# Optimization experiments

Measured on AMD Instinct MI355X. Metric: run time of the kernel, lower is better.

The kernel has to match this reference:

```python
import jax, jax.numpy as jnp
import numpy as np

N_EMBD = 2048
QKV_EMBD = 2048
N_HEAD = 32
N_KV_HEAD = 8
HEAD_DIM = QKV_EMBD // N_HEAD  # 64
GROUPS = N_HEAD // N_KV_HEAD   # 4
ROPE_THETA = 10000.0
SCALE = float(np.sqrt(HEAD_DIM))


def setup_inputs() -> dict:
    key = jax.random.key(0)
    ks = jax.random.split(key, 12)
    B, S = 2, 2048
    inp = {
        "query": jax.random.normal(ks[0], (B, S, N_EMBD), jnp.float32),
        "key": jax.random.normal(ks[1], (B, S, N_EMBD), jnp.float32),
        "value": jax.random.normal(ks[2], (B, S, N_EMBD), jnp.float32),
        "mask": jnp.ones((B, S), dtype=bool),
        "Wq": jax.random.normal(ks[3], (QKV_EMBD, N_EMBD), jnp.float32) * 0.02,
        "bq": jnp.zeros((QKV_EMBD,), jnp.float32),
        "Wk": jax.random.normal(ks[4], (N_KV_HEAD * HEAD_DIM, N_EMBD), jnp.float32) * 0.02,
        "bk": jnp.zeros((N_KV_HEAD * HEAD_DIM,), jnp.float32),
        "Wv": jax.random.normal(ks[5], (N_KV_HEAD * HEAD_DIM, N_EMBD), jnp.float32) * 0.02,
        "bv": jnp.zeros((N_KV_HEAD * HEAD_DIM,), jnp.float32),
        "Wo": jax.random.normal(ks[6], (N_EMBD, QKV_EMBD), jnp.float32) * 0.02,
        "bo": jnp.zeros((N_EMBD,), jnp.float32),
    }
    return inp


def _rotate_half(x):
    d = x.shape[-1] // 2
    return jnp.concatenate([-x[..., d:], x[..., :d]], axis=-1)


def _rope_cos_sin(seq_len, dtype):
    # rope_factor == 1.0 -> no NTK adjustment; is_causal -> position_ids = arange
    inv_freq = 1.0 / (ROPE_THETA ** (jnp.arange(0, HEAD_DIM, 2, dtype=jnp.float32) / HEAD_DIM))
    pos = jnp.arange(seq_len, dtype=jnp.float32)
    freqs = jnp.einsum("i,j->ij", pos, inv_freq)           # [S, D/2]
    emb = jnp.concatenate([freqs, freqs], axis=-1)          # [S, D]
    return jnp.cos(emb).astype(dtype)[None, None], jnp.sin(emb).astype(dtype)[None, None]


def reference(query, key, value, mask, Wq, bq, Wk, bk, Wv, bv, Wo, bo):
    B, S, _ = query.shape
    Q = (query @ Wq.T + bq).reshape(B, S, N_HEAD, HEAD_DIM).transpose(0, 2, 1, 3)      # [B,H,S,D]
    K = (key @ Wk.T + bk).reshape(B, S, N_KV_HEAD, HEAD_DIM).transpose(0, 2, 1, 3)     # [B,KV,S,D]
    V = (value @ Wv.T + bv).reshape(B, S, N_KV_HEAD, HEAD_DIM).transpose(0, 2, 1, 3)

    cos, sin = _rope_cos_sin(S, Q.dtype)
    Q = Q * cos + _rotate_half(Q) * sin
    K = K * cos + _rotate_half(K) * sin

    # interleaved GQA repeat: each kv head serves GROUPS consecutive query heads
    K = jnp.repeat(K, GROUPS, axis=1)  # [B,H,S,D]
    V = jnp.repeat(V, GROUPS, axis=1)

    attn = jnp.einsum("bhqd,bhkd->bhqk", Q, K)              # [B,H,S,S]
    causal = jnp.tril(jnp.ones((S, S), dtype=bool))
    full_mask = mask[:, None, None, :] & causal[None, None]  # [B,1,S,S]
    attn = jnp.where(full_mask, attn, jnp.finfo(attn.dtype).min)
    attn_weights = jax.nn.softmax(attn / SCALE, axis=-1)     # dropout p=0 (eval)
    out = jnp.einsum("bhqk,bhkd->bhqd", attn_weights, V)
    out = out.transpose(0, 2, 1, 3).reshape(B, S, QKV_EMBD)
    return out @ Wo.T + bo
```

## Files before the change

### kernel.cpp

```cpp
#include <hip/hip_runtime.h>
#include <hip/hip_bf16.h>
#include <cmath>

#define NE   2048
#define NH   32
#define NKV  8
#define HD   64
#define SEQ  2048
#define NB   2

typedef __attribute__((ext_vector_type(4))) float f32x4;
typedef __attribute__((ext_vector_type(16))) float f32x16;
typedef __attribute__((ext_vector_type(8))) short bf16x8;
typedef __attribute__((ext_vector_type(4))) short bf16x4;
typedef __attribute__((ext_vector_type(4))) unsigned u32x4;

typedef const __attribute__((address_space(1))) void cgvoid;
typedef __attribute__((address_space(3))) void lvoid;

#define QSCALE 0.18033688011112042f

__device__ __forceinline__ short f2bf(float f) {
  union { float f; unsigned u; } v; v.f = f;
  unsigned r = v.u + 0x7fffu + ((v.u >> 16) & 1u);
  return (short)(r >> 16);
}

__device__ __forceinline__ unsigned cvt_pk_bf16(float a, float b) {
  unsigned r;
  asm("v_cvt_pk_bf16_f32 %0, %1, %2" : "=v"(r) : "v"(a), "v"(b));
  return r;
}

__global__ __launch_bounds__(256) void cvt_w(
    const float* __restrict__ s0, short* __restrict__ d0,
    const float* __restrict__ s1, short* __restrict__ d1,
    const float* __restrict__ s2, short* __restrict__ d2,
    const float* __restrict__ s3, short* __restrict__ d3)
{
  int idx = blockIdx.x * 256 + threadIdx.x;
  const float* s; short* d; int rel;
  if      (idx < 524288)  { s = s0; d = d0; rel = idx; }
  else if (idx < 655360)  { s = s1; d = d1; rel = idx - 524288; }
  else if (idx < 786432)  { s = s2; d = d2; rel = idx - 655360; }
  else                    { s = s3; d = d3; rel = idx - 786432; }
  size_t off = (size_t)rel * 8;
  f32x4 a = *(const f32x4*)(s + off);
  f32x4 b = *(const f32x4*)(s + off + 4);
  bf16x8 o;
  #pragma unroll
  for (int j = 0; j < 4; ++j) { o[j] = f2bf(a[j]); o[4 + j] = f2bf(b[j]); }
  *(bf16x8*)(d + off) = o;
}

template<int EPI>
__device__ __forceinline__ void gemm256_body(
    short* As, short* Ws, int m0, int n0,
    const float* __restrict__ A, const short* __restrict__ W,
    const float* __restrict__ bias, void* __restrict__ Cout, int K)
{
  const int t = threadIdx.x, lane = t & 63, w = t >> 6;
  const int lr = lane & 15, lg = lane >> 4;
  const int wm = (w >> 2) * 128, wn = (w & 3) * 64;

  f32x4 acc[8][4];
  #pragma unroll
  for (int i = 0; i < 8; ++i)
    #pragma unroll
    for (int j = 0; j < 4; ++j) acc[i][j] = (f32x4){0.f, 0.f, 0.f, 0.f};

  auto STAGE_W = [&](int kt) {
    const int k0 = kt << 6;
    short* Wd = Ws + (kt & 1) * 16384;
    #pragma unroll
    for (int it = 0; it < 4; ++it) {
      int e = it * 512 + t, r = e >> 3, c = e & 7;
      int cs = ((c ^ (r & 7)) << 3);
      __builtin_amdgcn_global_load_lds((cgvoid*)(W + (size_t)(n0 + r) * K + k0 + cs),
                                       (lvoid*)(Wd + e * 8), 16, 0, 0);
    }
  };

  f32x4 areg[4][2];
  auto LOAD_A = [&](int kt) {
    const int k0 = kt << 6;
    #pragma unroll
    for (int it = 0; it < 4; ++it) {
      int e = it * 512 + t, r = e >> 3, c = e & 7;
      int cs = ((c ^ (r & 7)) << 3);
      const float* src = A + (size_t)(m0 + r) * K + k0 + cs;
      areg[it][0] = *(const f32x4*)(src);
      areg[it][1] = *(const f32x4*)(src + 4);
    }
  };
  auto WRITE_A = [&](int kt) {
    short* Ad = As + (kt & 1) * 16384;
    #pragma unroll
    for (int it = 0; it < 4; ++it) {
      int e = it * 512 + t;
      u32x4 v;
      v[0] = cvt_pk_bf16(areg[it][0][0], areg[it][0][1]);
      v[1] = cvt_pk_bf16(areg[it][0][2], areg[it][0][3]);
      v[2] = cvt_pk_bf16(areg[it][1][0], areg[it][1][1]);
      v[3] = cvt_pk_bf16(areg[it][1][2], areg[it][1][3]);
      *(u32x4*)(Ad + e * 8) = v;
    }
  };

  const int nt = K >> 6;

  STAGE_W(0);
  LOAD_A(0);
  WRITE_A(0);
  asm volatile("s_waitcnt lgkmcnt(0)" ::: "memory");

  for (int ti = 0; ti < nt; ++ti) {
    const short* Ab = As + (ti & 1) * 16384;
    const short* Wb = Ws + (ti & 1) * 16384;
    if (ti + 1 < nt) {
      STAGE_W(ti + 1);
      LOAD_A(ti + 1);
      asm volatile("s_waitcnt vmcnt(12)" ::: "memory");
    } else {
      asm volatile("s_waitcnt vmcnt(0)" ::: "memory");
    }
    __builtin_amdgcn_s_barrier();

    bf16x8 wf[2][4];
    #pragma unroll
    for (int ks = 0; ks < 2; ++ks)
      #pragma unroll
      for (int nf = 0; nf < 4; ++nf) {
        int row = wn + nf * 16 + lr;
        wf[ks][nf] = *(const bf16x8*)(Wb + row * 64 + (((ks * 4 + lg) ^ (row & 7)) << 3));
      }
    #pragma unroll
    for (int mq = 0; mq < 4; ++mq) {
      bf16x8 af[2][2];
      #pragma unroll
      for (int ks = 0; ks < 2; ++ks)
        #pragma unroll
        for (int mi = 0; mi < 2; ++mi) {
          int row = wm + (mq * 2 + mi) * 16 + lr;
          af[ks][mi] = *(const bf16x8*)(Ab + row * 64 + (((ks * 4 + lg) ^ (row & 7)) << 3));
        }
      __builtin_amdgcn_s_setprio(1);
      #pragma unroll
      for (int ks = 0; ks < 2; ++ks)
        #pragma unroll
        for (int mi = 0; mi < 2; ++mi)
          #pragma unroll
          for (int nf = 0; nf < 4; ++nf)
            acc[mq * 2 + mi][nf] =
                __builtin_amdgcn_mfma_f32_16x16x32_bf16(af[ks][mi], wf[ks][nf],
                                                        acc[mq * 2 + mi][nf], 0, 0, 0);
      __builtin_amdgcn_s_setprio(0);
    }
    if (ti + 1 < nt) WRITE_A(ti + 1);
    asm volatile("s_waitcnt lgkmcnt(0)" ::: "memory");
    __builtin_amdgcn_s_barrier();
  }

  if (EPI == 1) {
    short* C = (short*)Cout;
    #pragma unroll
    for (int mf = 0; mf < 8; ++mf)
      #pragma unroll
      for (int nf = 0; nf < 4; ++nf) {
        int n = n0 + wn + nf * 16 + lr;
        int kv = n >> 6, d = n & 63;
        int mb = m0 + wm + mf * 16 + lg * 4;
        int b = mb >> 11, s = mb & (SEQ - 1);
        bf16x4 pb;
        #pragma unroll
        for (int i = 0; i < 4; ++i) pb[i] = f2bf(acc[mf][nf][i] + bias[n]);
        *(bf16x4*)(C + (((size_t)b * NKV + kv) * HD + d) * SEQ + s) = pb;
      }
  } else {
    const int HN = (EPI == 2) ? NH : NKV;
    short* C = (short*)Cout;
    #pragma unroll
    for (int mf = 0; mf < 8; ++mf)
      #pragma unroll
      for (int nf2 = 0; nf2 < 2; ++nf2) {
        int n1 = n0 + wn + nf2 * 16 + lr;
        int d1 = n1 & 63;
        int h = n1 >> 6;
        float inv = exp2f(-(float)d1 * (13.287712379549449f / 32.0f));
        #pragma unroll
        for (int i = 0; i < 4; ++i) {
          int m = m0 + wm + mf * 16 + lg * 4 + i;
          int b = m >> 11, s = m & (SEQ - 1);
          float v1 = acc[mf][nf2][i] + bias[n1];
          float v2 = acc[mf][nf2 + 2][i] + bias[n1 + 32];
          float ang = (float)s * inv;
          float c, sn;
          __sincosf(ang, &sn, &c);
          float o1 = v1 * c - v2 * sn;
          float o2 = v2 * c + v1 * sn;
          if (EPI == 2) { o1 *= QSCALE; o2 *= QSCALE; }
          size_t base = (((size_t)b * HN + h) * SEQ + s) * HD;
          C[base + d1]      = f2bf(o1);
          C[base + d1 + 32] = f2bf(o2);
        }
      }
  }
}

__global__ __launch_bounds__(512, 2) void gemm_qkv256(
    const float* __restrict__ qA, const short* __restrict__ Wq,
    const float* __restrict__ bq, short* __restrict__ Qout,
    const float* __restrict__ kA, const short* __restrict__ Wk,
    const float* __restrict__ bk, short* __restrict__ Kout,
    const float* __restrict__ vA, const short* __restrict__ Wv,
    const float* __restrict__ bv, short* __restrict__ Vout)
{
  __shared__ __align__(16) short As[2 * 256 * 64];
  __shared__ __align__(16) short Ws[2 * 256 * 64];
  int orig = blockIdx.x;
  int bid = (orig & 7) * 24 + (orig >> 3);
  if (bid < 128) {
    gemm256_body<2>(As, Ws, (bid & 15) * 256, (bid >> 4) * 256, qA, Wq, bq, (void*)Qout, NE);
  } else if (bid < 160) {
    int b2 = bid - 128;
    gemm256_body<3>(As, Ws, (b2 & 15) * 256, (b2 >> 4) * 256, kA, Wk, bk, (void*)Kout, NE);
  } else {
    int b2 = bid - 160;
    gemm256_body<1>(As, Ws, (b2 & 15) * 256, (b2 >> 4) * 256, vA, Wv, bv, (void*)Vout, NE);
  }
}

__global__ __launch_bounds__(256) void gemm_o(
    const short* __restrict__ A, const short* __restrict__ W,
    const float* __restrict__ bias, float* __restrict__ C, int N, int K)
{
  __shared__ __align__(16) short As[2 * 128 * 64];
  __shared__ __align__(16) short Ws[2 * 128 * 64];
  const int t = threadIdx.x, lane = t & 63, w = t >> 6;
  const int lr = lane & 15, lg = lane >> 4;
  const int wm = (w >> 1) * 64, wn = (w & 1) * 64;
  const int L = blockIdx.x;
  const int xcd = L & 7, slot = L >> 3;
  const int bx = xcd + 8 * (slot >> 4);
  const int byy = slot & 15;
  const int m0 = bx * 128, n0 = byy * 128;

  f32x4 acc[4][4];
  #pragma unroll
  for (int i = 0; i < 4; ++i)
    #pragma unroll
    for (int j = 0; j < 4; ++j) acc[i][j] = (f32x4){0.f, 0.f, 0.f, 0.f};

  const int nt = K >> 6;
  #pragma unroll
  for (int it = 0; it < 4; ++it) {
    int e = it * 256 + t, r = e >> 3, c = e & 7;
    int cs = ((c ^ (r & 7)) << 3);
    __builtin_amdgcn_global_load_lds((cgvoid*)(A + (size_t)(m0 + r) * K + cs),
                                     (lvoid*)(As + e * 8), 16, 0, 0);
    __builtin_amdgcn_global_load_lds((cgvoid*)(W + (size_t)(n0 + r) * K + cs),
                                     (lvoid*)(Ws + e * 8), 16, 0, 0);
  }

  for (int ti = 0; ti < nt; ++ti) {
    const int cur = ti & 1;
    const short* Ab = As + cur * 8192;
    const short* Wb = Ws + cur * 8192;
    if (ti + 1 < nt) {
      const int k0 = (ti + 1) << 6;
      short* An = As + (cur ^ 1) * 8192;
      short* Wn = Ws + (cur ^ 1) * 8192;
      #pragma unroll
      for (int it = 0; it < 4; ++it) {
        int e = it * 256 + t, r = e >> 3, c = e & 7;
        int cs = ((c ^ (r & 7)) << 3);
        __builtin_amdgcn_global_load_lds((cgvoid*)(A + (size_t)(m0 + r) * K + k0 + cs),
                                         (lvoid*)(An + e * 8), 16, 0, 0);
        __builtin_amdgcn_global_load_lds((cgvoid*)(W + (size_t)(n0 + r) * K + k0 + cs),
                                         (lvoid*)(Wn + e * 8), 16, 0, 0);
      }
      asm volatile("s_waitcnt vmcnt(8)" ::: "memory");
    } else {
      asm volatile("s_waitcnt vmcnt(0)" ::: "memory");
    }
    __builtin_amdgcn_s_barrier();
    __builtin_amdgcn_sched_barrier(0);

    bf16x8 wf[2][4];
    #pragma unroll
    for (int ks = 0; ks < 2; ++ks)
      #pragma unroll
      for (int nf = 0; nf < 4; ++nf) {
        int row = wn + nf * 16 + lr;
        wf[ks][nf] = *(const bf16x8*)(Wb + row * 64 + (((ks * 4 + lg) ^ (row & 7)) << 3));
      }
    #pragma unroll
    for (int mq = 0; mq < 2; ++mq) {
      bf16x8 af[2][2];
      #pragma unroll
      for (int ks = 0; ks < 2; ++ks)
        #pragma unroll
        for (int mi = 0; mi < 2; ++mi) {
          int row = wm + (mq * 2 + mi) * 16 + lr;
          af[ks][mi] = *(const bf16x8*)(Ab + row * 64 + (((ks * 4 + lg) ^ (row & 7)) << 3));
        }
      __builtin_amdgcn_s_setprio(1);
      #pragma unroll
      for (int ks = 0; ks < 2; ++ks)
        #pragma unroll
        for (int mi = 0; mi < 2; ++mi)
          #pragma unroll
          for (int nf = 0; nf < 4; ++nf)
            acc[mq * 2 + mi][nf] =
                __builtin_amdgcn_mfma_f32_16x16x32_bf16(af[ks][mi], wf[ks][nf],
                                                        acc[mq * 2 + mi][nf], 0, 0, 0);
      __builtin_amdgcn_s_setprio(0);
      __builtin_amdgcn_s_barrier();
      __builtin_amdgcn_sched_barrier(0);
    }
  }

  #pragma unroll
  for (int mf = 0; mf < 4; ++mf)
    #pragma unroll
    for (int nf = 0; nf < 4; ++nf)
      #pragma unroll
      for (int i = 0; i < 4; ++i) {
        int m = m0 + wm + mf * 16 + lg * 4 + i;
        int n = n0 + wn + nf * 16 + lr;
        C[(size_t)m * N + n] = acc[mf][nf][i] + bias[n];
      }
}

__global__ __launch_bounds__(256) void attn_kernel(
    const short* __restrict__ Q, const short* __restrict__ K,
    const short* __restrict__ Vt, short* __restrict__ O)
{
  __shared__ __align__(16) short Ks[2][64 * 64];
  __shared__ __align__(16) short Vs[2][64 * 64];

  const int t = threadIdx.x, lane = t & 63, w = t >> 6;
  const int l31 = lane & 31, hi = lane >> 5;
  const int L = blockIdx.x;
  const int xcd = L & 7, slot = L >> 3;
  const int by = xcd + 8 * (slot >> 5);
  const int bx = slot & 31;
  const int b = by >> 3, kvh = by & 7;
  const int h = kvh * 4 + w;

  const short* Qh = Q + ((size_t)b * NH + h) * SEQ * HD;
  const short* Kh = K + ((size_t)b * NKV + kvh) * SEQ * HD;
  const short* Vh = Vt + ((size_t)b * NKV + kvh) * (size_t)HD * SEQ;

  #pragma unroll 1
  for (int pass = 0; pass < 2; ++pass) {
    const int qb32 = pass ? bx : (63 - bx);
    const int q0 = qb32 * 32;
    const int ntile = (qb32 >> 1) + 1;
    const int qpos = q0 + l31;

    bf16x8 qfr[4];
    #pragma unroll
    for (int dd = 0; dd < 4; ++dd)
      qfr[dd] = *(const bf16x8*)(Qh + (size_t)(q0 + l31) * HD + dd * 16 + hi * 8);

    f32x16 o[2];
    #pragma unroll
    for (int dh = 0; dh < 2; ++dh)
      #pragma unroll
      for (int r = 0; r < 16; ++r) o[dh][r] = 0.f;
    float lsum = 0.f;

    #pragma unroll
    for (int it = 0; it < 2; ++it) {
      int cid = it * 256 + t;
      int r = cid >> 3, c = cid & 7;
      int cs = ((c ^ (r & 7)) << 3);
      __builtin_amdgcn_global_load_lds((cgvoid*)(Kh + (size_t)r * HD + cs),
                                       (lvoid*)(Ks[0] + cid * 8), 16, 0, 0);
      __builtin_amdgcn_global_load_lds((cgvoid*)(Vh + (size_t)r * SEQ + cs),
                                       (lvoid*)(Vs[0] + cid * 8), 16, 0, 0);
    }
    __syncthreads();

    for (int ti = 0; ti < ntile; ++ti) {
      const int cur = ti & 1;
      if (ti + 1 < ntile) {
        const int kvn = (ti + 1) * 64;
        #pragma unroll
        for (int it = 0; it < 2; ++it) {
          int cid = it * 256 + t;
          int r = cid >> 3, c = cid & 7;
          int cs = ((c ^ (r & 7)) << 3);
          __builtin_amdgcn_global_load_lds((cgvoid*)(Kh + (size_t)(kvn + r) * HD + cs),
                                           (lvoid*)(Ks[cur ^ 1] + cid * 8), 16, 0, 0);
          __builtin_amdgcn_global_load_lds((cgvoid*)(Vh + (size_t)r * SEQ + kvn + cs),
                                           (lvoid*)(Vs[cur ^ 1] + cid * 8), 16, 0, 0);
        }
      }
      const int kv0 = ti * 64;
      const short* Kb = Ks[cur];
      const short* Vb = Vs[cur];

      f32x16 p[2];
      __builtin_amdgcn_s_setprio(1);
      #pragma unroll
      for (int f = 0; f < 2; ++f) {
        f32x16 z;
        #pragma unroll
        for (int r = 0; r < 16; ++r) z[r] = 0.f;
        #pragma unroll
        for (int dd = 0; dd < 4; ++dd) {
          int row = f * 32 + l31;
          bf16x8 ka = *(const bf16x8*)(Kb + row * 64 + (((2 * dd + hi) ^ (row & 7)) << 3));
          z = __builtin_amdgcn_mfma_f32_32x32x16_bf16(ka, qfr[dd], z, 0, 0, 0);
        }
        p[f] = z;
      }
      __builtin_amdgcn_s_setprio(0);

      if (ti == ntile - 1) {
        #pragma unroll
        for (int f = 0; f < 2; ++f)
          #pragma unroll
          for (int r = 0; r < 16; ++r) {
            int kpos = kv0 + f * 32 + (r & 3) + 8 * (r >> 2) + 4 * hi;
            if (kpos > qpos) p[f][r] = -INFINITY;
          }
      }

      unsigned pa[4][4];
      #pragma unroll
      for (int f = 0; f < 2; ++f) {
        float e[16];
        #pragma unroll
        for (int r = 0; r < 16; ++r) {
          e[r] = __builtin_amdgcn_exp2f(p[f][r]);
          lsum += e[r];
        }
        unsigned c[8];
        #pragma unroll
        for (int i = 0; i < 8; ++i) c[i] = cvt_pk_bf16(e[2 * i], e[2 * i + 1]);
        asm volatile("v_permlane32_swap_b32 %0, %1" : "+v"(c[0]), "+v"(c[2]));
        asm volatile("v_permlane32_swap_b32 %0, %1" : "+v"(c[1]), "+v"(c[3]));
        asm volatile("v_permlane32_swap_b32 %0, %1" : "+v"(c[4]), "+v"(c[6]));
        asm volatile("v_permlane32_swap_b32 %0, %1" : "+v"(c[5]), "+v"(c[7]));
        pa[2 * f][0] = c[0]; pa[2 * f][1] = c[1]; pa[2 * f][2] = c[2]; pa[2 * f][3] = c[3];
        pa[2 * f + 1][0] = c[4]; pa[2 * f + 1][1] = c[5];
        pa[2 * f + 1][2] = c[6]; pa[2 * f + 1][3] = c[7];
      }

      __builtin_amdgcn_s_setprio(1);
      #pragma unroll
      for (int ks = 0; ks < 4; ++ks) {
        bf16x8 paf = *(const bf16x8*)&pa[ks][0];
        #pragma unroll
        for (int dh = 0; dh < 2; ++dh) {
          int row = dh * 32 + l31;
          bf16x8 vb = *(const bf16x8*)(Vb + row * 64 + (((2 * ks + hi) ^ (row & 7)) << 3));
          o[dh] = __builtin_amdgcn_mfma_f32_32x32x16_bf16(paf, vb, o[dh], 0, 0, 0);
        }
      }
      __builtin_amdgcn_s_setprio(0);
      __syncthreads();
    }

    lsum += __shfl_xor(lsum, 32);
    #pragma unroll
    for (int r = 0; r < 16; ++r) {
      int crow = (r & 3) + 8 * (r >> 2) + 4 * hi;
      float li = __shfl(lsum, crow, 64);
      float invl = 1.0f / li;
      int s = q0 + crow;
      size_t base = (((size_t)b * SEQ + s) * NH + h) * HD;
      O[base + l31]      = f2bf(o[0][r] * invl);
      O[base + 32 + l31] = f2bf(o[1][r] * invl);
    }
  }
}

extern "C" void kernel_launch(void* const* d_in, const int* in_sizes, int n_in,
                              void* d_out, int out_size, void* d_ws, size_t ws_size,
                              hipStream_t stream) {
  (void)in_sizes; (void)n_in; (void)out_size; (void)ws_size;
  const float* q  = (const float*)d_in[0];
  const float* k  = (const float*)d_in[1];
  const float* v  = (const float*)d_in[2];
  const float* Wq = (const float*)d_in[4];
  const float* bq = (const float*)d_in[5];
  const float* Wk = (const float*)d_in[6];
  const float* bk = (const float*)d_in[7];
  const float* Wv = (const float*)d_in[8];
  const float* bv = (const float*)d_in[9];
  const float* Wo = (const float*)d_in[10];
  const float* bo = (const float*)d_in[11];

  const size_t SQ2 = (size_t)NB * SEQ * NE;
  const size_t W1  = (size_t)NE * NE;
  const size_t W2  = (size_t)(NKV * HD) * NE;
  const size_t KVN = (size_t)NB * NKV * SEQ * HD;

  short* ws = (short*)d_ws;
  short* Wqb = ws;
  short* Wkb = Wqb + W1;
  short* Wvb = Wkb + W2;
  short* Wob = Wvb + W2;
  short* Qr  = Wob + W1;
  short* Kr  = Qr + SQ2;
  short* Vr  = Kr + KVN;
  short* Ob  = Vr + KVN;

  dim3 blk(256);

  cvt_w<<<5120, blk, 0, stream>>>(Wq, Wqb, Wk, Wkb, Wv, Wvb, Wo, Wob);
  gemm_qkv256<<<192, dim3(512), 0, stream>>>(q, Wqb, bq, Qr, k, Wkb, bk, Kr, v, Wvb, bv, Vr);
  attn_kernel<<<512, blk, 0, stream>>>(Qr, Kr, Vr, Ob);
  gemm_o<<<512, blk, 0, stream>>>(Ob, Wob, bo, (float*)d_out, NE, NE);
}
```

Before: 192.6 us.

## Prefetch A tiles two iterations ahead with ping-pong register buffers

The GEMM main loop now loads the fp32 A tile two k-iterations ahead into one of two alternating register sets, while the bf16 conversion and LDS write use the other set. The loop is manually unrolled by two so the register roles swap without dynamic indexing. This is meant to hide global-load latency of A behind more MFMA work. It doubles the A staging registers, which may lower occupancy or cause spills. The vmcnt waits were adjusted to match the new load ordering.

```diff
diff --git a/kernel.cpp b/kernel.cpp
--- a/kernel.cpp
+++ b/kernel.cpp
@@ -81,51 +81,44 @@
     }
   };
 
-  f32x4 areg[4][2];
-  auto LOAD_A = [&](int kt) {
+  f32x4 rA[4][2], rB[4][2];
+  auto LOAD_A = [&](int kt, f32x4 (&ar)[4][2]) {
     const int k0 = kt << 6;
     #pragma unroll
     for (int it = 0; it < 4; ++it) {
       int e = it * 512 + t, r = e >> 3, c = e & 7;
       int cs = ((c ^ (r & 7)) << 3);
       const float* src = A + (size_t)(m0 + r) * K + k0 + cs;
-      areg[it][0] = *(const f32x4*)(src);
-      areg[it][1] = *(const f32x4*)(src + 4);
+      ar[it][0] = *(const f32x4*)(src);
+      ar[it][1] = *(const f32x4*)(src + 4);
     }
   };
-  auto WRITE_A = [&](int kt) {
+  auto WRITE_A = [&](int kt, f32x4 (&ar)[4][2]) {
     short* Ad = As + (kt & 1) * 16384;
     #pragma unroll
     for (int it = 0; it < 4; ++it) {
       int e = it * 512 + t;
       u32x4 v;
-      v[0] = cvt_pk_bf16(areg[it][0][0], areg[it][0][1]);
-      v[1] = cvt_pk_bf16(areg[it][0][2], areg[it][0][3]);
-      v[2] = cvt_pk_bf16(areg[it][1][0], areg[it][1][1]);
-      v[3] = cvt_pk_bf16(areg[it][1][2], areg[it][1][3]);
+      v[0] = cvt_pk_bf16(ar[it][0][0], ar[it][0][1]);
+      v[1] = cvt_pk_bf16(ar[it][0][2], ar[it][0][3]);
+      v[2] = cvt_pk_bf16(ar[it][1][0], ar[it][1][1]);
+      v[3] = cvt_pk_bf16(ar[it][1][2], ar[it][1][3]);
       *(u32x4*)(Ad + e * 8) = v;
     }
   };
 
   const int nt = K >> 6;
 
-  STAGE_W(0);
-  LOAD_A(0);
-  WRITE_A(0);
-  asm volatile("s_waitcnt lgkmcnt(0)" ::: "memory");
-
-  for (int ti = 0; ti < nt; ++ti) {
-    const short* Ab = As + (ti & 1) * 16384;
-    const short* Wb = Ws + (ti & 1) * 16384;
-    if (ti + 1 < nt) {
-      STAGE_W(ti + 1);
-      LOAD_A(ti + 1);
-      asm volatile("s_waitcnt vmcnt(12)" ::: "memory");
-    } else {
-      asm volatile("s_waitcnt vmcnt(0)" ::: "memory");
-    }
+  auto ITER = [&](int tt, f32x4 (&SC)[4][2], f32x4 (&SO)[4][2]) {
+    if (tt + 2 < nt) LOAD_A(tt + 2, SC);
+    if (tt + 1 < nt) STAGE_W(tt + 1);
+    if (tt + 2 < nt)      { asm volatile("s_waitcnt vmcnt(12)" ::: "memory"); }
+    else if (tt + 1 < nt) { asm volatile("s_waitcnt vmcnt(4)"  ::: "memory"); }
+    else                  { asm volatile("s_waitcnt vmcnt(0)"  ::: "memory"); }
     __builtin_amdgcn_s_barrier();
 
+    const short* Ab = As + (tt & 1) * 16384;
+    const short* Wb = Ws + (tt & 1) * 16384;
     bf16x8 wf[2][4];
     #pragma unroll
     for (int ks = 0; ks < 2; ++ks)
@@ -156,9 +149,21 @@
                                                         acc[mq * 2 + mi][nf], 0, 0, 0);
       __builtin_amdgcn_s_setprio(0);
     }
-    if (ti + 1 < nt) WRITE_A(ti + 1);
+    if (tt + 1 < nt) WRITE_A(tt + 1, SO);
     asm volatile("s_waitcnt lgkmcnt(0)" ::: "memory");
     __builtin_amdgcn_s_barrier();
+  };
+
+  LOAD_A(0, rA);
+  LOAD_A(1, rB);
+  STAGE_W(0);
+  WRITE_A(0, rA);
+  asm volatile("s_waitcnt lgkmcnt(0)" ::: "memory");
+
+  #pragma unroll 1
+  for (int ti = 0; ti < nt; ti += 2) {
+    ITER(ti,     rA, rB);
+    ITER(ti + 1, rB, rA);
   }
 
   if (EPI == 1) {
```

Result: slower. 299.9 us (+55.7%).
